# Kernel tuning notes

Hardware: AMD Instinct MI355X
Metric: run time of the kernel (lower is better)

## Reference

```python
import jax, jax.numpy as jnp
import numpy as np

N, T, E, H, V = 32768, 20, 50, 50, 200
PAD = 0

def setup_inputs() -> dict:
    key = jax.random.key(0)
    ks = jax.random.split(key, 11)
    s = 1.0 / np.sqrt(H)  # torch LSTM init scale
    return {
        "char_indices": jax.random.randint(ks[0], (N, T), 0, V, dtype=jnp.int32),
        "word_lengths": jax.random.randint(ks[1], (N,), 0, T + 1, dtype=jnp.int32),
        "emb": jax.random.normal(ks[2], (V, E), jnp.float32) * 0.1,
        "W_ih_f": jax.random.normal(ks[3], (4 * H, E), jnp.float32) * s,
        "W_hh_f": jax.random.normal(ks[4], (4 * H, H), jnp.float32) * s,
        "b_ih_f": jax.random.normal(ks[5], (4 * H,), jnp.float32) * s,
        "b_hh_f": jax.random.normal(ks[6], (4 * H,), jnp.float32) * s,
        "W_ih_b": jax.random.normal(ks[7], (4 * H, E), jnp.float32) * s,
        "W_hh_b": jax.random.normal(ks[8], (4 * H, H), jnp.float32) * s,
        "b_ih_b": jax.random.normal(ks[9], (4 * H,), jnp.float32) * s,
        "b_hh_b": jax.random.normal(ks[10], (4 * H,), jnp.float32) * s,
    }

def _run_dir(x, lengths, W_ih, W_hh, b_ih, b_hh, reverse):
    # x: [N,T,E]; returns final hidden state [N,H] at the word's true boundary.
    n = x.shape[0]
    xg = jnp.einsum('nte,ge->ntg', x, W_ih) + b_ih + b_hh  # [N,T,4H]
    def step(carry, t):
        h, c = carry
        g = xg[:, t] + h @ W_hh.T  # [N,4H]
        i, f, gg, o = jnp.split(g, 4, axis=-1)
        c_new = jax.nn.sigmoid(f) * c + jax.nn.sigmoid(i) * jnp.tanh(gg)
        h_new = jax.nn.sigmoid(o) * jnp.tanh(c_new)
        valid = (t < lengths)[:, None]  # only update inside the word
        return (jnp.where(valid, h_new, h), jnp.where(valid, c_new, c)), None
    ts = jnp.arange(T - 1, -1, -1) if reverse else jnp.arange(T)
    z = jnp.zeros((n, W_hh.shape[1]), x.dtype)
    (h, _), _ = jax.lax.scan(step, (z, z), ts)
    return h

def reference(char_indices, word_lengths, emb, W_ih_f, W_hh_f, b_ih_f, b_hh_f,
              W_ih_b, W_hh_b, b_ih_b, b_hh_b):
    emb = emb.at[PAD].set(0.0)  # padding_idx row is zero
    x = emb[char_indices]  # [N,T,E]
    h_f = _run_dir(x, word_lengths, W_ih_f, W_hh_f, b_ih_f, b_hh_f, reverse=False)
    h_b = _run_dir(x, word_lengths, W_ih_b, W_hh_b, b_ih_b, b_hh_b, reverse=True)
    return jnp.concatenate([h_f, h_b], axis=-1)  # [N, 2H]
```

## Files before the change

### kernel.cpp

```cpp
#include <hip/hip_runtime.h>


#define TT    20
#define HH    50
#define VV    200
#define TILES 13
#define GSTR  212
#define GSH   (VV * GSTR)
#define WSH   (TILES * 16 * 64)
#define NW    32768
#define NB_G  332
#define NB_W  104
#define NB_H  128

typedef __attribute__((ext_vector_type(8))) short bf16x8;
typedef __attribute__((ext_vector_type(4))) short s16x4;
typedef __attribute__((ext_vector_type(4))) float f32x4;

__device__ __forceinline__ float frcp(float x) { return __builtin_amdgcn_rcpf(x); }
__device__ __forceinline__ float fsig(float x) { return frcp(1.0f + __expf(-x)); }
__device__ __forceinline__ float ftanhf(float x) { return 1.0f - 2.0f * frcp(1.0f + __expf(2.0f * x)); }

__device__ __forceinline__ short f2bf(float x) {
    unsigned b = __builtin_bit_cast(unsigned, x);
    unsigned r = (b + 0x7FFFu + ((b >> 16) & 1u)) >> 16;
    return (short)r;
}
__device__ __forceinline__ float bf2f(short s) {
    return __builtin_bit_cast(float, ((unsigned)(unsigned short)s) << 16);
}

__global__ void k_prep(const float* __restrict__ emb,
                       const float* __restrict__ Wih_f, const float* __restrict__ bih_f,
                       const float* __restrict__ bhh_f,
                       const float* __restrict__ Wih_b, const float* __restrict__ bih_b,
                       const float* __restrict__ bhh_b,
                       const float* __restrict__ Whh_f, const float* __restrict__ Whh_b,
                       const int* __restrict__ lens,
                       short* __restrict__ Gimg, short* __restrict__ Wimg,
                       int* __restrict__ cnt) {
    int blk = blockIdx.x;
    int tid = threadIdx.x;
    if (blk < NB_G) {
        int idx = blk * 256 + tid;
        if (idx >= 2 * GSH) return;
        int d = idx / GSH;
        int rem = idx % GSH;
        int v = rem / GSTR;
        int u = (rem % GSTR) >> 2;
        int g = idx & 3;
        if (u >= HH) { Gimg[idx] = 0; return; }
        int r = g * HH + u;
        const float* Wih = d ? Wih_b : Wih_f;
        const float* bih = d ? bih_b : bih_f;
        const float* bhh = d ? bhh_b : bhh_f;
        float s = bih[r] + bhh[r];
        if (v != 0) {
            #pragma unroll 10
            for (int e = 0; e < HH; ++e) s = fmaf(emb[v * HH + e], Wih[r * HH + e], s);
        }
        Gimg[idx] = f2bf(s);
    } else if (blk < NB_G + NB_W) {
        int idx = (blk - NB_G) * 256 + tid;
        if (idx >= 2 * WSH) return;
        int d = idx / WSH;
        int e = idx % WSH;
        int t = e >> 10, m = (e >> 6) & 15, k = e & 63;
        int u = 4 * t + (m >> 2), g = m & 3;
        const float* Whh = d ? Whh_b : Whh_f;
        float val = (k < HH && u < HH) ? Whh[(g * HH + u) * HH + k] : 0.0f;
        int ksw = (k & 7) | (((k >> 3) ^ (m & 7)) << 3);
        Wimg[d * WSH + (e & ~63) + ksw] = f2bf(val);
    } else {
        int hb = blk - NB_G - NB_W;
        __shared__ int hcnt[21];
        if (tid < 21) hcnt[tid] = 0;
        __syncthreads();
        atomicAdd(&hcnt[lens[hb * 256 + tid]], 1);
        __syncthreads();
        if (tid < 21) cnt[hb * 21 + tid] = hcnt[tid];
    }
}

__global__ void k_scan(const int* __restrict__ cnt, int* __restrict__ offs) {
    __shared__ int tot[21], start[21];
    int t = threadIdx.x;
    if (t < 21) {
        int s = 0;
        for (int b = 0; b < NB_H; ++b) s += cnt[b * 21 + t];
        tot[t] = s;
    }
    __syncthreads();
    if (t == 0) {
        int acc = 0;
        for (int L = 20; L >= 0; --L) { start[L] = acc; acc += tot[L]; }
    }
    __syncthreads();
    if (t < 21) {
        int acc = start[t];
        for (int b = 0; b < NB_H; ++b) { offs[b * 21 + t] = acc; acc += cnt[b * 21 + t]; }
    }
}

__global__ void k_scat(const int* __restrict__ lens, const int* __restrict__ offs,
                       int* __restrict__ perm) {
    __shared__ int cur[21];
    int b = blockIdx.x, t = threadIdx.x;
    if (t < 21) cur[t] = offs[b * 21 + t];
    __syncthreads();
    int i = b * 256 + t;
    int pos = atomicAdd(&cur[lens[i]], 1);
    perm[pos] = i;
}

__launch_bounds__(512, 1)
__global__ void k_lstm(const int* __restrict__ chars, const int* __restrict__ lens,
                       const int* __restrict__ perm,
                       const short* __restrict__ Gimg, const short* __restrict__ Wimg,
                       float* __restrict__ out) {
    __shared__ __align__(16) short Wa[WSH];
    __shared__ __align__(16) short Gl[GSH];
    __shared__ __align__(16) short hs[8][1024];
    __shared__ unsigned char cs[8][320];

    int gb   = blockIdx.x;
    int d    = gb & 1;
    int grp  = gb >> 1;
    int tid  = threadIdx.x;
    int lane = tid & 63;
    int wv   = __builtin_amdgcn_readfirstlane(tid >> 6);
    int quad = lane >> 4;
    int n    = lane & 15;
    int x7   = n & 7;

    {
        const int4* src = (const int4*)(Wimg + d * WSH);
        int4* dst = (int4*)Wa;
        for (int i = tid; i < WSH / 8; i += 512) dst[i] = src[i];
    }
    {
        const int4* src = (const int4*)(Gimg + d * GSH);
        int4* dst = (int4*)Gl;
        for (int i = tid; i < GSH / 8; i += 512) dst[i] = src[i];
    }
    {
        int4 z = {0, 0, 0, 0};
        int4* hz = (int4*)&hs[0][0];
        for (int i = tid; i < 8 * 1024 / 8; i += 512) hz[i] = z;
    }
    int slotbase = (grp * 8 + wv) * 16;
    {
        for (int i = lane; i < 16 * TT; i += 64) {
            int w = perm[slotbase + i / TT];
            cs[wv][i] = (unsigned char)chars[w * TT + i % TT];
        }
    }
    __syncthreads();

    int word = perm[slotbase + n];
    int L = lens[word];
    int mL = L;
    #pragma unroll
    for (int off = 8; off; off >>= 1) {
        int t2 = __shfl_xor(mL, off);
        mL = mL > t2 ? mL : t2;
    }
    mL = __builtin_amdgcn_readfirstlane(mL);

    const bf16x8* ap = (const bf16x8*)Wa;
    const bf16x8* bp = (const bf16x8*)hs[wv];
    short* hw = hs[wv];
    const unsigned char* cw = cs[wv] + n * TT;

    int pa0 = quad ^ x7;
    int pa1 = (quad + 4) ^ x7;

    float cst[TILES], hf[TILES];
    #pragma unroll
    for (int t = 0; t < TILES; ++t) { cst[t] = 0.0f; hf[t] = 0.0f; }

    #pragma unroll 1
    for (int s = 0; s < mL; ++s) {
        bool valid = s < L;
        int p = valid ? (d ? (L - 1 - s) : s) : 0;
        int v = cw[p];

        bf16x8 B0 = bp[n * 8 + pa0];
        bf16x8 B1 = bp[n * 8 + pa1];

        f32x4 acc[TILES];
        #pragma unroll
        for (int t = 0; t < TILES; ++t) {
            int u = 4 * t + quad;
            s16x4 gv = *(const s16x4*)&Gl[v * GSTR + u * 4];
            f32x4 a;
            a[0] = bf2f(gv[0]); a[1] = bf2f(gv[1]);
            a[2] = bf2f(gv[2]); a[3] = bf2f(gv[3]);
            bf16x8 A0 = ap[(t * 16 + n) * 8 + pa0];
            bf16x8 A1 = ap[(t * 16 + n) * 8 + pa1];
            a = __builtin_amdgcn_mfma_f32_16x16x32_bf16(A0, B0, a, 0, 0, 0);
            a = __builtin_amdgcn_mfma_f32_16x16x32_bf16(A1, B1, a, 0, 0, 0);
            acc[t] = a;
        }
        #pragma unroll
        for (int t = 0; t < TILES; ++t) {
            int u = 4 * t + quad;
            float ig = fsig(acc[t][0]);
            float fg = fsig(acc[t][1]);
            float gg = ftanhf(acc[t][2]);
            float og = fsig(acc[t][3]);
            float cold = cst[t];
            float cn = fg * cold + ig * gg;
            float hn = og * ftanhf(cn);
            bool upd = valid && (u < HH);
            cst[t] = upd ? cn : cold;
            hf[t]  = upd ? hn : hf[t];
            if (upd) {
                int idx = n * 64 + (((u >> 3) ^ x7) << 3) + (u & 7);
                hw[idx] = f2bf(hn);
            }
        }
    }

    float* orow = out + (size_t)word * (2 * HH) + d * HH;
    #pragma unroll
    for (int t = 0; t < TILES; ++t) {
        int u = 4 * t + quad;
        if (u < HH) orow[u] = hf[t];
    }
}

extern "C" void kernel_launch(void* const* d_in, const int* in_sizes, int n_in,
                              void* d_out, int out_size, void* d_ws, size_t ws_size,
                              hipStream_t stream) {
    const int*   chars = (const int*)d_in[0];
    const int*   lens  = (const int*)d_in[1];
    const float* emb   = (const float*)d_in[2];
    const float* Wih_f = (const float*)d_in[3];
    const float* Whh_f = (const float*)d_in[4];
    const float* bih_f = (const float*)d_in[5];
    const float* bhh_f = (const float*)d_in[6];
    const float* Wih_b = (const float*)d_in[7];
    const float* Whh_b = (const float*)d_in[8];
    const float* bih_b = (const float*)d_in[9];
    const float* bhh_b = (const float*)d_in[10];
    float* out = (float*)d_out;

    short* Gimg = (short*)d_ws;
    short* Wimg = Gimg + 2 * GSH;
    int*   cnt  = (int*)(Wimg + 2 * WSH);
    int*   offs = cnt + NB_H * 21;
    int*   perm = offs + NB_H * 21;

    k_prep<<<NB_G + NB_W + NB_H, 256, 0, stream>>>(emb, Wih_f, bih_f, bhh_f,
                                                   Wih_b, bih_b, bhh_b,
                                                   Whh_f, Whh_b, lens,
                                                   Gimg, Wimg, cnt);
    k_scan<<<1, 64, 0, stream>>>(cnt, offs);
    k_scat<<<NB_H, 256, 0, stream>>>(lens, offs, perm);
    k_lstm<<<512, 512, 0, stream>>>(chars, lens, perm, Gimg, Wimg, out);
}
```

Measured before the change: 159.9 us.

## Drop LDS gate table, prescale weights for exp2, parallelize scan, raise occupancy

The per-character gate table moves out of LDS and is read from global memory, with the next character's index prefetched one step ahead. This cuts LDS use per block so launch bounds can ask for four blocks per CU. Gate weights and biases are prescaled by -log2e (and 2·log2e for the tanh gate), so the activations use raw exp2 without an extra multiply. The step is split into two halves to lower register pressure, blocks are remapped so long and short words pair up, and the offset scan is spread over 168 threads. The gate table now comes from L2/global memory on each step, which may add latency, and asking for higher occupancy may cause register spills.

```diff
diff --git a/kernel.cpp b/kernel.cpp
--- a/kernel.cpp
+++ b/kernel.cpp
@@ -13,13 +13,20 @@
 #define NB_W  104
 #define NB_H  128
 
+#define LOG2E   1.4426950408889634f
+#define N2LOG2E (-1.4426950408889634f)
+#define P2LOG2E 2.8853900817779268f
+
 typedef __attribute__((ext_vector_type(8))) short bf16x8;
 typedef __attribute__((ext_vector_type(4))) short s16x4;
 typedef __attribute__((ext_vector_type(4))) float f32x4;
 
 __device__ __forceinline__ float frcp(float x) { return __builtin_amdgcn_rcpf(x); }
-__device__ __forceinline__ float fsig(float x) { return frcp(1.0f + __expf(-x)); }
-__device__ __forceinline__ float ftanhf(float x) { return 1.0f - 2.0f * frcp(1.0f + __expf(2.0f * x)); }
+#if __has_builtin(__builtin_amdgcn_exp2f)
+__device__ __forceinline__ float fexp2(float x) { return __builtin_amdgcn_exp2f(x); }
+#else
+__device__ __forceinline__ float fexp2(float x) { return exp2f(x); }
+#endif
 
 __device__ __forceinline__ short f2bf(float x) {
     unsigned b = __builtin_bit_cast(unsigned, x);
@@ -59,7 +66,8 @@
             #pragma unroll 10
             for (int e = 0; e < HH; ++e) s = fmaf(emb[v * HH + e], Wih[r * HH + e], s);
         }
-        Gimg[idx] = f2bf(s);
+        float sc = (g == 2) ? P2LOG2E : N2LOG2E;
+        Gimg[idx] = f2bf(s * sc);
     } else if (blk < NB_G + NB_W) {
         int idx = (blk - NB_G) * 256 + tid;
         if (idx >= 2 * WSH) return;
@@ -68,7 +76,8 @@
         int t = e >> 10, m = (e >> 6) & 15, k = e & 63;
         int u = 4 * t + (m >> 2), g = m & 3;
         const float* Whh = d ? Whh_b : Whh_f;
-        float val = (k < HH && u < HH) ? Whh[(g * HH + u) * HH + k] : 0.0f;
+        float sc = (g == 2) ? P2LOG2E : N2LOG2E;
+        float val = (k < HH && u < HH) ? Whh[(g * HH + u) * HH + k] * sc : 0.0f;
         int ksw = (k & 7) | (((k >> 3) ^ (m & 7)) << 3);
         Wimg[d * WSH + (e & ~63) + ksw] = f2bf(val);
     } else {
@@ -83,22 +92,35 @@
 }
 
 __global__ void k_scan(const int* __restrict__ cnt, int* __restrict__ offs) {
+    __shared__ int part[8][21];
     __shared__ int tot[21], start[21];
     int t = threadIdx.x;
+    int L = t % 21, c = t / 21;
+    if (t < 168) {
+        int s = 0;
+        for (int b = c * 16; b < c * 16 + 16; ++b) s += cnt[b * 21 + L];
+        part[c][L] = s;
+    }
+    __syncthreads();
     if (t < 21) {
-        int s = 0;
-        for (int b = 0; b < NB_H; ++b) s += cnt[b * 21 + t];
-        tot[t] = s;
+        int a = 0;
+        #pragma unroll
+        for (int c2 = 0; c2 < 8; ++c2) a += part[c2][t];
+        tot[t] = a;
     }
     __syncthreads();
     if (t == 0) {
         int acc = 0;
-        for (int L = 20; L >= 0; --L) { start[L] = acc; acc += tot[L]; }
-    }
-    __syncthreads();
-    if (t < 21) {
-        int acc = start[t];
-        for (int b = 0; b < NB_H; ++b) { offs[b * 21 + t] = acc; acc += cnt[b * 21 + t]; }
+        for (int Lq = 20; Lq >= 0; --Lq) { start[Lq] = acc; acc += tot[Lq]; }
+    }
+    __syncthreads();
+    if (t < 168) {
+        int base = start[L];
+        for (int c2 = 0; c2 < c; ++c2) base += part[c2][L];
+        for (int b = c * 16; b < c * 16 + 16; ++b) {
+            offs[b * 21 + L] = base;
+            base += cnt[b * 21 + L];
+        }
     }
 }
 
@@ -113,19 +135,19 @@
     perm[pos] = i;
 }
 
-__launch_bounds__(512, 1)
+__launch_bounds__(512, 4)
 __global__ void k_lstm(const int* __restrict__ chars, const int* __restrict__ lens,
                        const int* __restrict__ perm,
                        const short* __restrict__ Gimg, const short* __restrict__ Wimg,
                        float* __restrict__ out) {
     __shared__ __align__(16) short Wa[WSH];
-    __shared__ __align__(16) short Gl[GSH];
     __shared__ __align__(16) short hs[8][1024];
     __shared__ unsigned char cs[8][320];
 
     int gb   = blockIdx.x;
-    int d    = gb & 1;
-    int grp  = gb >> 1;
+    int rank = (gb < 256) ? gb : (767 - gb);
+    int d    = rank & 1;
+    int grp  = rank >> 1;
     int tid  = threadIdx.x;
     int lane = tid & 63;
     int wv   = __builtin_amdgcn_readfirstlane(tid >> 6);
@@ -139,21 +161,14 @@
         for (int i = tid; i < WSH / 8; i += 512) dst[i] = src[i];
     }
     {
-        const int4* src = (const int4*)(Gimg + d * GSH);
-        int4* dst = (int4*)Gl;
-        for (int i = tid; i < GSH / 8; i += 512) dst[i] = src[i];
-    }
-    {
         int4 z = {0, 0, 0, 0};
         int4* hz = (int4*)&hs[0][0];
         for (int i = tid; i < 8 * 1024 / 8; i += 512) hz[i] = z;
     }
     int slotbase = (grp * 8 + wv) * 16;
-    {
-        for (int i = lane; i < 16 * TT; i += 64) {
-            int w = perm[slotbase + i / TT];
-            cs[wv][i] = (unsigned char)chars[w * TT + i % TT];
-        }
+    for (int i = lane; i < 16 * TT; i += 64) {
+        int w = perm[slotbase + i / TT];
+        cs[wv][i] = (unsigned char)chars[w * TT + i % TT];
     }
     __syncthreads();
 
@@ -171,6 +186,7 @@
     const bf16x8* bp = (const bf16x8*)hs[wv];
     short* hw = hs[wv];
     const unsigned char* cw = cs[wv] + n * TT;
+    const short* Gg = Gimg + d * GSH;
 
     int pa0 = quad ^ x7;
     int pa1 = (quad + 4) ^ x7;
@@ -179,45 +195,59 @@
     #pragma unroll
     for (int t = 0; t < TILES; ++t) { cst[t] = 0.0f; hf[t] = 0.0f; }
 
+    int p0 = d ? (L > 0 ? L - 1 : 0) : 0;
+    int vcur = cw[p0];
+
     #pragma unroll 1
     for (int s = 0; s < mL; ++s) {
         bool valid = s < L;
-        int p = valid ? (d ? (L - 1 - s) : s) : 0;
-        int v = cw[p];
+
+        const short* gvp = Gg + vcur * GSTR + quad * 4;
+        s16x4 gv[TILES];
+        #pragma unroll
+        for (int t = 0; t < TILES; ++t) gv[t] = *(const s16x4*)(gvp + t * 16);
 
         bf16x8 B0 = bp[n * 8 + pa0];
         bf16x8 B1 = bp[n * 8 + pa1];
 
-        f32x4 acc[TILES];
+        int sn = s + 1;
+        int pn = (sn < L) ? (d ? (L - 1 - sn) : sn) : 0;
+        vcur = cw[pn];
+
         #pragma unroll
-        for (int t = 0; t < TILES; ++t) {
-            int u = 4 * t + quad;
-            s16x4 gv = *(const s16x4*)&Gl[v * GSTR + u * 4];
-            f32x4 a;
-            a[0] = bf2f(gv[0]); a[1] = bf2f(gv[1]);
-            a[2] = bf2f(gv[2]); a[3] = bf2f(gv[3]);
-            bf16x8 A0 = ap[(t * 16 + n) * 8 + pa0];
-            bf16x8 A1 = ap[(t * 16 + n) * 8 + pa1];
-            a = __builtin_amdgcn_mfma_f32_16x16x32_bf16(A0, B0, a, 0, 0, 0);
-            a = __builtin_amdgcn_mfma_f32_16x16x32_bf16(A1, B1, a, 0, 0, 0);
-            acc[t] = a;
-        }
-        #pragma unroll
-        for (int t = 0; t < TILES; ++t) {
-            int u = 4 * t + quad;
-            float ig = fsig(acc[t][0]);
-            float fg = fsig(acc[t][1]);
-            float gg = ftanhf(acc[t][2]);
-            float og = fsig(acc[t][3]);
-            float cold = cst[t];
-            float cn = fg * cold + ig * gg;
-            float hn = og * ftanhf(cn);
-            bool upd = valid && (u < HH);
-            cst[t] = upd ? cn : cold;
-            hf[t]  = upd ? hn : hf[t];
-            if (upd) {
-                int idx = n * 64 + (((u >> 3) ^ x7) << 3) + (u & 7);
-                hw[idx] = f2bf(hn);
+        for (int half = 0; half < 2; ++half) {
+            const int t0 = half ? 7 : 0;
+            const int t1 = half ? TILES : 7;
+            f32x4 acc[7];
+            #pragma unroll
+            for (int t = t0; t < t1; ++t) {
+                f32x4 a;
+                a[0] = bf2f(gv[t][0]); a[1] = bf2f(gv[t][1]);
+                a[2] = bf2f(gv[t][2]); a[3] = bf2f(gv[t][3]);
+                bf16x8 A0 = ap[(t * 16 + n) * 8 + pa0];
+                bf16x8 A1 = ap[(t * 16 + n) * 8 + pa1];
+                a = __builtin_amdgcn_mfma_f32_16x16x32_bf16(A0, B0, a, 0, 0, 0);
+                a = __builtin_amdgcn_mfma_f32_16x16x32_bf16(A1, B1, a, 0, 0, 0);
+                acc[t - t0] = a;
+            }
+            #pragma unroll
+            for (int t = t0; t < t1; ++t) {
+                f32x4 a = acc[t - t0];
+                int u = 4 * t + quad;
+                float ig = frcp(1.0f + fexp2(a[0]));
+                float fg = frcp(1.0f + fexp2(a[1]));
+                float tg = 1.0f - 2.0f * frcp(1.0f + fexp2(a[2]));
+                float og = frcp(1.0f + fexp2(a[3]));
+                float cold = cst[t];
+                float cn = fg * cold + ig * tg;
+                float hn = og * (1.0f - 2.0f * frcp(1.0f + fexp2(cn * P2LOG2E)));
+                bool upd = valid && (u < HH);
+                cst[t] = upd ? cn : cold;
+                hf[t]  = upd ? hn : hf[t];
+                if (upd) {
+                    int idx = n * 64 + (((u >> 3) ^ x7) << 3) + (u & 7);
+                    hw[idx] = f2bf(hn);
+                }
             }
         }
     }
@@ -256,7 +286,7 @@
                                                    Wih_b, bih_b, bhh_b,
                                                    Whh_f, Whh_b, lens,
                                                    Gimg, Wimg, cnt);
-    k_scan<<<1, 64, 0, stream>>>(cnt, offs);
+    k_scan<<<1, 256, 0, stream>>>(cnt, offs);
     k_scat<<<NB_H, 256, 0, stream>>>(lens, offs, perm);
     k_lstm<<<512, 512, 0, stream>>>(chars, lens, perm, Gimg, Wimg, out);
 }
```

Measured after the change: 299.7 us. 87.4% more time.
